# Kernel optimization log

Measured on AMD Instinct MI355X. Metric: run time of the kernel, lower is better.

## Reference

```python
import jax, jax.numpy as jnp
import numpy as np

S, B, H, V, T = 128, 64, 512, 100, 32  # src_len, batch, hidden, vocab, tgt_len


def setup_inputs() -> dict:
    key = jax.random.key(0)
    ks = jax.random.split(key, 12)
    sc = 0.05
    return {
        "encoder_outputs": jax.random.normal(ks[0], (S, B, H), jnp.float32),
        "W_emb": jax.random.normal(ks[1], (V, H), jnp.float32) * sc,   # embedding.weight.T (Linear(V->H, no bias) on one-hot)
        "W_comb": jax.random.normal(ks[2], (H, 2 * H), jnp.float32) * sc,
        "b_comb": jnp.zeros((H,), jnp.float32),
        "W_ih": jax.random.normal(ks[3], (3 * H, H), jnp.float32) * sc,
        "W_hh": jax.random.normal(ks[4], (3 * H, H), jnp.float32) * sc,
        "b_ih": jnp.zeros((3 * H,), jnp.float32),
        "b_hh": jnp.zeros((3 * H,), jnp.float32),
        "W_out": jax.random.normal(ks[5], (V, H), jnp.float32) * sc,
        "b_out": jnp.zeros((V,), jnp.float32),
        "w_vat": jax.random.normal(ks[6], (H,), jnp.float32) * sc,     # vat: Linear(H->1)
        "b_vat": jnp.zeros((), jnp.float32),
        "target_seq": jax.random.randint(ks[7], (T, B), 0, V),
    }


def reference(encoder_outputs, W_emb, W_comb, b_comb, W_ih, W_hh, b_ih, b_hh,
              W_out, b_out, w_vat, b_vat, target_seq):
    # train_forward with teacher forcing, dropout in eval (identity).
    def step(h, sym):  # h: [B,H], sym: [B] int
        embedded = W_emb[sym]                                   # one-hot @ embedding.weight.T
        # Bahdanau additive attention: scores over src positions
        scores = jnp.tanh(encoder_outputs + h[None]) @ w_vat + b_vat   # [S,B]
        attn = jax.nn.softmax(scores, axis=0)                   # softmax over S
        ctx = jnp.einsum('sb,sbh->bh', attn, encoder_outputs)   # [B,H]
        x = jax.nn.relu(jnp.concatenate([embedded, ctx], axis=-1) @ W_comb.T + b_comb)
        # PyTorch GRU cell
        gi = x @ W_ih.T + b_ih                                   # [B,3H]
        gh = h @ W_hh.T + b_hh
        ir, iz, inn = jnp.split(gi, 3, axis=-1)
        hr, hz, hn = jnp.split(gh, 3, axis=-1)
        r = jax.nn.sigmoid(ir + hr)
        z = jax.nn.sigmoid(iz + hz)
        n = jnp.tanh(inn + r * hn)
        h_new = (1.0 - z) * n + z * h
        logits = jax.nn.log_softmax(h_new @ W_out.T + b_out, axis=-1)  # [B,V]
        return h_new, logits

    h0 = jnp.zeros((encoder_outputs.shape[1], W_hh.shape[1]), encoder_outputs.dtype)
    _, logits = jax.lax.scan(step, h0, target_seq[:-1])          # [T-1,B,V]
    return jnp.transpose(logits, (1, 0, 2))                      # [B,T-1,V]
```

## Files before the change

### kernel.cpp

```cpp
#include <hip/hip_runtime.h>
#include <hip/hip_fp16.h>

#define Sn 128
#define Bn 64
#define Hn 512
#define Vn 100
#define TSn 31

typedef unsigned int   u32;
typedef unsigned short u16;
typedef _Float16 f16x2 __attribute__((ext_vector_type(2)));

#define OFF_ENC2  0ull
#define OFF_WEMB  8388608ull
#define OFF_WCOMB 8491008ull
#define OFF_WIH   9539584ull
#define OFF_WHH   11112448ull
#define OFF_WOUT  12685312ull
#define OFF_XEX   12787712ull
#define OFF_HEX   12853248ull
#define OFF_HHEX  12984320ull
#define OFF_PLOG  13049856ull
#define OFF_CNT   13152256ull

__device__ __forceinline__ u16 f2h(float f){ _Float16 h=(_Float16)f; return __builtin_bit_cast(u16,h); }
__device__ __forceinline__ f16x2 uh2(u32 u){ return __builtin_bit_cast(f16x2,u); }
__device__ __forceinline__ float2 h2f(u32 u){ f16x2 h=uh2(u); return make_float2((float)h.x,(float)h.y); }
__device__ __forceinline__ u32 pack2h(float a, float b){ return (u32)f2h(a) | ((u32)f2h(b) << 16); }

#if __has_builtin(__builtin_amdgcn_fdot2)
__device__ __forceinline__ float dot2acc(u32 a, u32 b, float acc){
    return __builtin_amdgcn_fdot2(uh2(a), uh2(b), acc, false);
}
#else
__device__ __forceinline__ float dot2acc(u32 a, u32 b, float acc){
    float2 x=h2f(a), y=h2f(b); return acc + x.x*y.x + x.y*y.y;
}
#endif

__device__ __forceinline__ float dot8h(uint4 w, uint4 v, float acc){
    acc = dot2acc(w.x, v.x, acc); acc = dot2acc(w.y, v.y, acc);
    acc = dot2acc(w.z, v.z, acc); acc = dot2acc(w.w, v.w, acc);
    return acc;
}

__device__ __forceinline__ float fast_tanh(float x){
    float e = __expf(2.0f*x);
    return 1.0f - 2.0f/(e + 1.0f);
}
__device__ __forceinline__ float fast_sigmoid(float x){ return 1.0f/(1.0f + __expf(-x)); }

__device__ __forceinline__ float wave_sum(float v){
#pragma unroll
    for (int o = 32; o; o >>= 1) v += __shfl_xor(v, o);
    return v;
}
__device__ __forceinline__ float wave_max(float v){
#pragma unroll
    for (int o = 32; o; o >>= 1) v = fmaxf(v, __shfl_xor(v, o));
    return v;
}

__device__ __forceinline__ void sib_barrier(u32* cnt, u32 target){
    asm volatile("s_waitcnt vmcnt(0)" ::: "memory");
    __syncthreads();
    if (threadIdx.x == 0) {
        __hip_atomic_fetch_add(cnt, 1u, __ATOMIC_RELAXED, __HIP_MEMORY_SCOPE_AGENT);
        u32 v;
        do {
            __builtin_amdgcn_s_sleep(2);
            v = __hip_atomic_load(cnt, __ATOMIC_RELAXED, __HIP_MEMORY_SCOPE_AGENT);
        } while (v < target);
    }
    __syncthreads();
}

#define CONV(S,D,N)                                              \
    for (int i = t0; i < (N)/4; i += stride) {                   \
        float4 v = ((const float4*)(S))[i];                      \
        ushort4 o;                                               \
        o.x = f2h(v.x); o.y = f2h(v.y);                          \
        o.z = f2h(v.z); o.w = f2h(v.w);                          \
        ((ushort4*)(D))[i] = o;                                  \
    }

__global__ __launch_bounds__(256) void conv_f16(
    const float* __restrict__ enc, const float* __restrict__ Wemb,
    const float* __restrict__ Wcomb, const float* __restrict__ Wih,
    const float* __restrict__ Whh, const float* __restrict__ Wout,
    char* __restrict__ ws)
{
    const int t0 = blockIdx.x*256 + threadIdx.x;
    const int stride = gridDim.x*256;
    if (blockIdx.x == 0 && threadIdx.x < 128) ((u32*)(ws + OFF_CNT))[threadIdx.x] = 0;

    {
        u16* de = (u16*)(ws + OFF_ENC2);
        for (int c = t0; c < Sn*Bn*Hn/4; c += stride) {
            const int h4 = c & 127;
            const int s  = (c >> 7) & 127;
            const int bb = c >> 14;
            float4 v = ((const float4*)enc)[(s*Bn + bb)*(Hn/4) + h4];
            ushort4 o;
            o.x = f2h(v.x); o.y = f2h(v.y); o.z = f2h(v.z); o.w = f2h(v.w);
            ((ushort4*)de)[c] = o;
        }
    }
    u16* dm = (u16*)(ws + OFF_WEMB);
    u16* dc = (u16*)(ws + OFF_WCOMB);
    u16* di = (u16*)(ws + OFF_WIH);
    u16* dh = (u16*)(ws + OFF_WHH);
    u16* doo = (u16*)(ws + OFF_WOUT);
    CONV(Wemb, dm, Vn*Hn)
    CONV(Wcomb,dc, Hn*2*Hn)
    CONV(Wih,  di, 3*Hn*Hn)
    CONV(Whh,  dh, 3*Hn*Hn)
    CONV(Wout, doo, Vn*Hn)
}

__global__ __launch_bounds__(1024) void bahdanau_decoder(
    const float* __restrict__ bcomb, const float* __restrict__ bih,
    const float* __restrict__ bhh, const float* __restrict__ bout,
    const float* __restrict__ wvat, const float* __restrict__ bvat,
    const int* __restrict__ tgt, float* __restrict__ out, char* __restrict__ ws)
{
    const u16* Wemb_h  = (const u16*)(ws + OFF_WEMB);
    const u16* Wcomb_h = (const u16*)(ws + OFF_WCOMB);
    const u16* Wih_h   = (const u16*)(ws + OFF_WIH);
    const u16* Whh_h   = (const u16*)(ws + OFF_WHH);
    const u16* Wout_h  = (const u16*)(ws + OFF_WOUT);
    u32* cntA = (u32*)(ws + OFF_CNT);
    u32* cntB = cntA + 64;

    extern __shared__ __align__(16) u16 enc_lds[];
    __shared__ __align__(16) float h_full[Hn];
    __shared__ __align__(16) u16   hh_full[Hn];
    __shared__ __align__(16) u16   ec_s[2*Hn];
    __shared__ __align__(16) u16   x_s[Hn];
    __shared__ __align__(16) float scores_s[Sn];
    __shared__ __align__(16) float attnw_s[Sn];
    __shared__ __align__(16) float2 pctx[4][256];
    __shared__ __align__(16) float plog_s[112];
    __shared__ __align__(16) u16   hn16_stage[128];

    const int tid  = threadIdx.x;
    const int lane = tid & 63;
    const int wid  = tid >> 6;
    const int bid  = blockIdx.x;
    const int xcd  = bid & 7;
    const int lb   = bid >> 3;
    const int q    = xcd & 3;
    const int b    = 2*lb + (xcd >> 2);
    const int j0   = q*128;

    {
        const uint4* src = (const uint4*)(ws + OFF_ENC2 + (size_t)b*Sn*Hn*2);
        for (int i = tid; i < Sn*Hn/8; i += 1024) ((uint4*)enc_lds)[i] = src[i];
    }
    if (tid < Hn) { h_full[tid] = 0.0f; hh_full[tid] = 0; }
    const float4 Wa = ((const float4*)wvat)[2*lane];
    const float4 Wb = ((const float4*)wvat)[2*lane+1];
    const float bv = bvat[0];
    __syncthreads();

    for (int t = 0; t < TSn; ++t) {
        const u32 tgtc = 4u*(t+1);

        for (int s = wid; s < Sn; s += 16) {
            const uint4 E = ((const uint4*)(enc_lds + s*Hn))[lane];
            const float4 Ha = ((const float4*)h_full)[2*lane];
            const float4 Hb = ((const float4*)h_full)[2*lane+1];
            const float2 e0 = h2f(E.x), e1 = h2f(E.y), e2 = h2f(E.z), e3 = h2f(E.w);
            float acc = fast_tanh(e0.x+Ha.x)*Wa.x + fast_tanh(e0.y+Ha.y)*Wa.y
                      + fast_tanh(e1.x+Ha.z)*Wa.z + fast_tanh(e1.y+Ha.w)*Wa.w
                      + fast_tanh(e2.x+Hb.x)*Wb.x + fast_tanh(e2.y+Hb.y)*Wb.y
                      + fast_tanh(e3.x+Hb.z)*Wb.z + fast_tanh(e3.y+Hb.w)*Wb.w;
            acc = wave_sum(acc);
            if (lane == 0) scores_s[s] = acc + bv;
        }
        __syncthreads();

        if (wid == 0) {
            const float s0 = scores_s[lane], s1 = scores_s[lane+64];
            const float mx = wave_max(fmaxf(s0, s1));
            const float e0 = __expf(s0-mx), e1 = __expf(s1-mx);
            const float inv = 1.0f / wave_sum(e0 + e1);
            attnw_s[lane]    = e0 * inv;
            attnw_s[lane+64] = e1 * inv;
        } else if (wid == 1) {
            const int sym = tgt[t*Bn + b];
            ((uint4*)ec_s)[lane] = ((const uint4*)(Wemb_h + (size_t)sym*Hn))[lane];
        }
        __syncthreads();

        {
            const int op = tid & 255;
            const int sc = tid >> 8;
            float2 acc = make_float2(0.f, 0.f);
#pragma unroll 8
            for (int k = 0; k < 32; ++k) {
                const int s = sc*32 + k;
                const float2 ef = h2f(*(const u32*)(enc_lds + s*Hn + 2*op));
                const float a = attnw_s[s];
                acc.x += a*ef.x; acc.y += a*ef.y;
            }
            pctx[sc][op] = acc;
        }
        __syncthreads();
        if (tid < 256) {
            float2 c0 = pctx[0][tid], c1 = pctx[1][tid], c2 = pctx[2][tid], c3 = pctx[3][tid];
            ((u32*)(ec_s + Hn))[tid] = pack2h(c0.x+c1.x+c2.x+c3.x, c0.y+c1.y+c2.y+c3.y);
        }
        __syncthreads();

        for (int jj = wid; jj < 128; jj += 16) {
            const int j = j0 + jj;
            const uint4* row = (const uint4*)(Wcomb_h + (size_t)j*2*Hn);
            const uint4 w0 = row[lane], w1 = row[64+lane];
            const uint4 e0 = ((const uint4*)ec_s)[lane], e1 = ((const uint4*)ec_s)[64+lane];
            float acc = dot8h(w1, e1, dot8h(w0, e0, 0.0f));
            acc = wave_sum(acc);
            if (lane == 0) x_s[j] = f2h(fmaxf(acc + bcomb[j], 0.0f));
        }
        __syncthreads();
        if (wid == 0)
            ((volatile u32*)(ws + OFF_XEX))[b*256 + q*64 + lane] = ((u32*)x_s)[q*64 + lane];
        sib_barrier(cntA + b, tgtc);
        if (wid < 3) {
            const int qq = (q + 1 + wid) & 3;
            ((u32*)x_s)[qq*64 + lane] = ((const volatile u32*)(ws + OFF_XEX))[b*256 + qq*64 + lane];
        }
        __syncthreads();

        for (int jj = wid; jj < 128; jj += 16) {
            const int j = j0 + jj;
            const uint4 Wr = ((const uint4*)(Wih_h + (size_t)j*Hn))[lane];
            const uint4 Wz = ((const uint4*)(Wih_h + (size_t)(Hn + j)*Hn))[lane];
            const uint4 Wn = ((const uint4*)(Wih_h + (size_t)(2*Hn + j)*Hn))[lane];
            const uint4 Ur = ((const uint4*)(Whh_h + (size_t)j*Hn))[lane];
            const uint4 Uz = ((const uint4*)(Whh_h + (size_t)(Hn + j)*Hn))[lane];
            const uint4 Un = ((const uint4*)(Whh_h + (size_t)(2*Hn + j)*Hn))[lane];
            const uint4 Xv = ((const uint4*)x_s)[lane];
            const uint4 Hv = ((const uint4*)hh_full)[lane];
            float gr = dot8h(Ur, Hv, dot8h(Wr, Xv, 0.0f));
            float gz = dot8h(Uz, Hv, dot8h(Wz, Xv, 0.0f));
            float an = dot8h(Wn, Xv, 0.0f);
            float cn = dot8h(Un, Hv, 0.0f);
            gr = wave_sum(gr); gz = wave_sum(gz);
            an = wave_sum(an); cn = wave_sum(cn);
            if (lane == 0) {
                const float r = fast_sigmoid(gr + bih[j]      + bhh[j]);
                const float z = fast_sigmoid(gz + bih[Hn+j]   + bhh[Hn+j]);
                const float n = fast_tanh(an + bih[2*Hn+j] + r*(cn + bhh[2*Hn+j]));
                const float hv = (1.0f - z)*n + z*h_full[j];
                h_full[j] = hv;
                hn16_stage[jj] = f2h(hv);
            }
        }
        __syncthreads();

        for (int v = wid; v < Vn; v += 16) {
            const u32 w = *(const u32*)(Wout_h + (size_t)v*Hn + j0 + 2*lane);
            const u32 hh = ((u32*)hn16_stage)[lane];
            float acc = dot2acc(w, hh, 0.0f);
            acc = wave_sum(acc);
            if (lane == 0) plog_s[v] = acc;
        }
        __syncthreads();

        if (wid == 0) {
            if (lane < 50) {
                volatile float* pp = (volatile float*)(ws + OFF_PLOG) + ((size_t)b*4 + q)*100;
                pp[2*lane]   = plog_s[2*lane];
                pp[2*lane+1] = plog_s[2*lane+1];
            }
        } else if (wid == 1) {
            volatile float* hp = (volatile float*)(ws + OFF_HEX) + (size_t)b*Hn + j0;
            hp[2*lane]   = h_full[j0 + 2*lane];
            hp[2*lane+1] = h_full[j0 + 2*lane + 1];
        } else if (wid == 2) {
            ((volatile u32*)(ws + OFF_HHEX))[b*256 + q*64 + lane] = ((u32*)hn16_stage)[lane];
        }
        sib_barrier(cntB + b, tgtc);
        if (wid < 3) {
            const int qq = (q + 1 + wid) & 3;
            const volatile float* hp = (const volatile float*)(ws + OFF_HEX) + (size_t)b*Hn + qq*128;
            h_full[qq*128 + 2*lane]     = hp[2*lane];
            h_full[qq*128 + 2*lane + 1] = hp[2*lane+1];
            ((u32*)hh_full)[qq*64 + lane] = ((const volatile u32*)(ws + OFF_HHEX))[b*256 + qq*64 + lane];
        } else if (wid == 3) {
            ((u32*)hh_full)[q*64 + lane] = ((u32*)hn16_stage)[lane];
        } else if (wid == 4 && q == 0) {
            float a0 = 0.f, a1 = 0.f;
            if (lane < 50) {
                a0 = plog_s[2*lane] + bout[2*lane];
                a1 = plog_s[2*lane+1] + bout[2*lane+1];
#pragma unroll
                for (int qq = 1; qq < 4; ++qq) {
                    const volatile float* pp = (const volatile float*)(ws + OFF_PLOG) + ((size_t)b*4 + qq)*100;
                    a0 += pp[2*lane];
                    a1 += pp[2*lane+1];
                }
            }
            const float l0 = (lane < 50) ? a0 : -3.0e38f;
            const float l1 = (lane < 50) ? a1 : -3.0e38f;
            const float mx = wave_max(fmaxf(l0, l1));
            const float e0 = (lane < 50) ? __expf(l0-mx) : 0.0f;
            const float e1 = (lane < 50) ? __expf(l1-mx) : 0.0f;
            const float lse = mx + __logf(wave_sum(e0 + e1));
            float* op = out + ((size_t)b*TSn + t)*Vn;
            if (lane < 50) { op[2*lane] = l0 - lse; op[2*lane+1] = l1 - lse; }
        }
        __syncthreads();
    }
}

extern "C" void kernel_launch(void* const* d_in, const int* in_sizes, int n_in,
                              void* d_out, int out_size, void* d_ws, size_t ws_size,
                              hipStream_t stream) {
    const float* enc   = (const float*)d_in[0];
    const float* Wemb  = (const float*)d_in[1];
    const float* Wcomb = (const float*)d_in[2];
    const float* bcomb = (const float*)d_in[3];
    const float* Wih   = (const float*)d_in[4];
    const float* Whh   = (const float*)d_in[5];
    const float* bih   = (const float*)d_in[6];
    const float* bhh   = (const float*)d_in[7];
    const float* Wout  = (const float*)d_in[8];
    const float* bout  = (const float*)d_in[9];
    const float* wvat  = (const float*)d_in[10];
    const float* bvat  = (const float*)d_in[11];
    const int*   tgt   = (const int*)d_in[12];
    float* out = (float*)d_out;
    char*  ws  = (char*)d_ws;

    conv_f16<<<1024, 256, 0, stream>>>(enc, Wemb, Wcomb, Wih, Whh, Wout, ws);

    void* args[] = { &bcomb, &bih, &bhh, &bout, &wvat, &bvat, &tgt, &out, &ws };
    hipLaunchCooperativeKernel((const void*)bahdanau_decoder,
                               dim3(256), dim3(1024), args, (size_t)(Sn*Hn*2), stream);
}
```

Before: 1.218 ms.

## Precompute embedding-combine table and overlap W_hh gates with sibling barrier

Folds the embedding half of W_comb into a precomputed fp32 table, Wemb projected through W_comb, built by a new prep kernel, so each step only does a 512-wide context dot plus a table lookup. Splits the sibling barrier into arrive and wait, and computes the W_hh·h gate dot products between them so that work overlaps the cross-block wait. Also pads the counters onto separate cache lines, uses relaxed atomics instead of volatile for exchange traffic, and shortens the spin sleep. This adds an extra prep kernel and more register pressure from the held gate partials.

```diff
diff --git a/kernel.cpp b/kernel.cpp
--- a/kernel.cpp
+++ b/kernel.cpp
@@ -12,16 +12,16 @@
 typedef _Float16 f16x2 __attribute__((ext_vector_type(2)));
 
 #define OFF_ENC2  0ull
-#define OFF_WEMB  8388608ull
-#define OFF_WCOMB 8491008ull
-#define OFF_WIH   9539584ull
-#define OFF_WHH   11112448ull
-#define OFF_WOUT  12685312ull
-#define OFF_XEX   12787712ull
-#define OFF_HEX   12853248ull
-#define OFF_HHEX  12984320ull
-#define OFF_PLOG  13049856ull
-#define OFF_CNT   13152256ull
+#define OFF_WC2   8388608ull
+#define OFF_WIH   8912896ull
+#define OFF_WHH   10485760ull
+#define OFF_WOUT  12058624ull
+#define OFF_EMB2  12161024ull
+#define OFF_XEX   12365824ull
+#define OFF_HEXF  12431360ull
+#define OFF_HEXH  12562432ull
+#define OFF_PLOG  12627968ull
+#define OFF_CNT   12730368ull
 
 __device__ __forceinline__ u16 f2h(float f){ _Float16 h=(_Float16)f; return __builtin_bit_cast(u16,h); }
 __device__ __forceinline__ f16x2 uh2(u32 u){ return __builtin_bit_cast(f16x2,u); }
@@ -61,16 +61,29 @@
     return v;
 }
 
-__device__ __forceinline__ void sib_barrier(u32* cnt, u32 target){
+__device__ __forceinline__ void ast(u32* p, u32 v){
+    __hip_atomic_store(p, v, __ATOMIC_RELAXED, __HIP_MEMORY_SCOPE_AGENT);
+}
+__device__ __forceinline__ u32 ald(u32* p){
+    return __hip_atomic_load(p, __ATOMIC_RELAXED, __HIP_MEMORY_SCOPE_AGENT);
+}
+__device__ __forceinline__ void astf(float* p, float v){
+    __hip_atomic_store((u32*)p, __builtin_bit_cast(u32, v), __ATOMIC_RELAXED, __HIP_MEMORY_SCOPE_AGENT);
+}
+__device__ __forceinline__ float aldf(float* p){
+    return __builtin_bit_cast(float, __hip_atomic_load((u32*)p, __ATOMIC_RELAXED, __HIP_MEMORY_SCOPE_AGENT));
+}
+
+__device__ __forceinline__ void sib_arrive(u32* cnt){
     asm volatile("s_waitcnt vmcnt(0)" ::: "memory");
     __syncthreads();
+    if (threadIdx.x == 0)
+        __hip_atomic_fetch_add(cnt, 1u, __ATOMIC_RELAXED, __HIP_MEMORY_SCOPE_AGENT);
+}
+__device__ __forceinline__ void sib_wait(u32* cnt, u32 target){
     if (threadIdx.x == 0) {
-        __hip_atomic_fetch_add(cnt, 1u, __ATOMIC_RELAXED, __HIP_MEMORY_SCOPE_AGENT);
-        u32 v;
-        do {
-            __builtin_amdgcn_s_sleep(2);
-            v = __hip_atomic_load(cnt, __ATOMIC_RELAXED, __HIP_MEMORY_SCOPE_AGENT);
-        } while (v < target);
+        while (__hip_atomic_load(cnt, __ATOMIC_RELAXED, __HIP_MEMORY_SCOPE_AGENT) < target)
+            __builtin_amdgcn_s_sleep(1);
     }
     __syncthreads();
 }
@@ -84,16 +97,13 @@
         ((ushort4*)(D))[i] = o;                                  \
     }
 
-__global__ __launch_bounds__(256) void conv_f16(
-    const float* __restrict__ enc, const float* __restrict__ Wemb,
-    const float* __restrict__ Wcomb, const float* __restrict__ Wih,
-    const float* __restrict__ Whh, const float* __restrict__ Wout,
-    char* __restrict__ ws)
+__global__ __launch_bounds__(256) void prep_conv(
+    const float* __restrict__ enc, const float* __restrict__ Wcomb,
+    const float* __restrict__ Wih, const float* __restrict__ Whh,
+    const float* __restrict__ Wout, char* __restrict__ ws)
 {
     const int t0 = blockIdx.x*256 + threadIdx.x;
     const int stride = gridDim.x*256;
-    if (blockIdx.x == 0 && threadIdx.x < 128) ((u32*)(ws + OFF_CNT))[threadIdx.x] = 0;
-
     {
         u16* de = (u16*)(ws + OFF_ENC2);
         for (int c = t0; c < Sn*Bn*Hn/4; c += stride) {
@@ -106,16 +116,45 @@
             ((ushort4*)de)[c] = o;
         }
     }
-    u16* dm = (u16*)(ws + OFF_WEMB);
-    u16* dc = (u16*)(ws + OFF_WCOMB);
-    u16* di = (u16*)(ws + OFF_WIH);
-    u16* dh = (u16*)(ws + OFF_WHH);
-    u16* doo = (u16*)(ws + OFF_WOUT);
-    CONV(Wemb, dm, Vn*Hn)
-    CONV(Wcomb,dc, Hn*2*Hn)
-    CONV(Wih,  di, 3*Hn*Hn)
-    CONV(Whh,  dh, 3*Hn*Hn)
-    CONV(Wout, doo, Vn*Hn)
+    {
+        u16* dc = (u16*)(ws + OFF_WC2);
+        for (int i = t0; i < Hn*Hn/4; i += stride) {
+            const int j = i >> 7, kk = i & 127;
+            float4 v = ((const float4*)Wcomb)[j*256 + 128 + kk];
+            ushort4 o;
+            o.x = f2h(v.x); o.y = f2h(v.y); o.z = f2h(v.z); o.w = f2h(v.w);
+            ((ushort4*)dc)[i] = o;
+        }
+    }
+    CONV(Wih,  (u16*)(ws+OFF_WIH),  3*Hn*Hn)
+    CONV(Whh,  (u16*)(ws+OFF_WHH),  3*Hn*Hn)
+    CONV(Wout, (u16*)(ws+OFF_WOUT), Vn*Hn)
+    u32* cnt = (u32*)(ws + OFF_CNT);
+    for (int i = t0; i < 64*2*16; i += stride) cnt[i] = 0u;
+}
+
+__global__ __launch_bounds__(512) void prep_emb2(
+    const float* __restrict__ Wemb, const float* __restrict__ Wcomb,
+    char* __restrict__ ws)
+{
+    float* EMB2 = (float*)(ws + OFF_EMB2);
+    const int w = threadIdx.x >> 6;
+    const int lane = threadIdx.x & 63;
+    const int j = blockIdx.x*8 + w;
+    const float4* wc = (const float4*)(Wcomb + (size_t)j*2*Hn);
+#pragma unroll
+    for (int pass = 0; pass < 2; ++pass) {
+        const int v = lane + 64*pass;
+        if (v < Vn) {
+            const float4* we = (const float4*)(Wemb + (size_t)v*Hn);
+            float acc = 0.0f;
+            for (int k4 = 0; k4 < 128; ++k4) {
+                const float4 a = wc[k4], b = we[k4];
+                acc += a.x*b.x + a.y*b.y + a.z*b.z + a.w*b.w;
+            }
+            EMB2[(size_t)v*Hn + j] = acc;
+        }
+    }
 }
 
 __global__ __launch_bounds__(1024) void bahdanau_decoder(
@@ -124,24 +163,28 @@
     const float* __restrict__ wvat, const float* __restrict__ bvat,
     const int* __restrict__ tgt, float* __restrict__ out, char* __restrict__ ws)
 {
-    const u16* Wemb_h  = (const u16*)(ws + OFF_WEMB);
-    const u16* Wcomb_h = (const u16*)(ws + OFF_WCOMB);
-    const u16* Wih_h   = (const u16*)(ws + OFF_WIH);
-    const u16* Whh_h   = (const u16*)(ws + OFF_WHH);
-    const u16* Wout_h  = (const u16*)(ws + OFF_WOUT);
-    u32* cntA = (u32*)(ws + OFF_CNT);
-    u32* cntB = cntA + 64;
+    const u16* WC2  = (const u16*)(ws + OFF_WC2);
+    const u16* WIH  = (const u16*)(ws + OFF_WIH);
+    const u16* WHH  = (const u16*)(ws + OFF_WHH);
+    const u16* WOUT = (const u16*)(ws + OFF_WOUT);
+    const float* EMB2 = (const float*)(ws + OFF_EMB2);
+    u32*   XEX  = (u32*)(ws + OFF_XEX);
+    float* HEXF = (float*)(ws + OFF_HEXF);
+    u32*   HEXH = (u32*)(ws + OFF_HEXH);
+    float* PLOG = (float*)(ws + OFF_PLOG);
+    u32*   CNT  = (u32*)(ws + OFF_CNT);
 
     extern __shared__ __align__(16) u16 enc_lds[];
     __shared__ __align__(16) float h_full[Hn];
-    __shared__ __align__(16) u16   hh_full[Hn];
-    __shared__ __align__(16) u16   ec_s[2*Hn];
-    __shared__ __align__(16) u16   x_s[Hn];
+    __shared__ __align__(16) u32   hh32[Hn/2];
+    __shared__ __align__(16) u32   ctx32[Hn/2];
+    __shared__ __align__(16) u32   x32[Hn/2];
+    __shared__ __align__(16) u16   xst[128];
+    __shared__ __align__(16) u16   hn16[128];
     __shared__ __align__(16) float scores_s[Sn];
     __shared__ __align__(16) float attnw_s[Sn];
-    __shared__ __align__(16) float2 pctx[4][256];
+    __shared__ __align__(16) float2 pctx_s[4][256];
     __shared__ __align__(16) float plog_s[112];
-    __shared__ __align__(16) u16   hn16_stage[128];
 
     const int tid  = threadIdx.x;
     const int lane = tid & 63;
@@ -152,12 +195,15 @@
     const int q    = xcd & 3;
     const int b    = 2*lb + (xcd >> 2);
     const int j0   = q*128;
+    u32* cntA = CNT + (b*2 + 0)*16;
+    u32* cntB = CNT + (b*2 + 1)*16;
 
     {
         const uint4* src = (const uint4*)(ws + OFF_ENC2 + (size_t)b*Sn*Hn*2);
         for (int i = tid; i < Sn*Hn/8; i += 1024) ((uint4*)enc_lds)[i] = src[i];
     }
-    if (tid < Hn) { h_full[tid] = 0.0f; hh_full[tid] = 0; }
+    if (tid < Hn) h_full[tid] = 0.0f;
+    if (tid < Hn/2) hh32[tid] = 0u;
     const float4 Wa = ((const float4*)wvat)[2*lane];
     const float4 Wb = ((const float4*)wvat)[2*lane+1];
     const float bv = bvat[0];
@@ -166,17 +212,19 @@
     for (int t = 0; t < TSn; ++t) {
         const u32 tgtc = 4u*(t+1);
 
-        for (int s = wid; s < Sn; s += 16) {
-            const uint4 E = ((const uint4*)(enc_lds + s*Hn))[lane];
+        {
             const float4 Ha = ((const float4*)h_full)[2*lane];
             const float4 Hb = ((const float4*)h_full)[2*lane+1];
-            const float2 e0 = h2f(E.x), e1 = h2f(E.y), e2 = h2f(E.z), e3 = h2f(E.w);
-            float acc = fast_tanh(e0.x+Ha.x)*Wa.x + fast_tanh(e0.y+Ha.y)*Wa.y
-                      + fast_tanh(e1.x+Ha.z)*Wa.z + fast_tanh(e1.y+Ha.w)*Wa.w
-                      + fast_tanh(e2.x+Hb.x)*Wb.x + fast_tanh(e2.y+Hb.y)*Wb.y
-                      + fast_tanh(e3.x+Hb.z)*Wb.z + fast_tanh(e3.y+Hb.w)*Wb.w;
-            acc = wave_sum(acc);
-            if (lane == 0) scores_s[s] = acc + bv;
+            for (int s = wid; s < Sn; s += 16) {
+                const uint4 E = ((const uint4*)(enc_lds + s*Hn))[lane];
+                const float2 e0 = h2f(E.x), e1 = h2f(E.y), e2 = h2f(E.z), e3 = h2f(E.w);
+                float acc = fast_tanh(e0.x+Ha.x)*Wa.x + fast_tanh(e0.y+Ha.y)*Wa.y
+                          + fast_tanh(e1.x+Ha.z)*Wa.z + fast_tanh(e1.y+Ha.w)*Wa.w
+                          + fast_tanh(e2.x+Hb.x)*Wb.x + fast_tanh(e2.y+Hb.y)*Wb.y
+                          + fast_tanh(e3.x+Hb.z)*Wb.z + fast_tanh(e3.y+Hb.w)*Wb.w;
+                acc = wave_sum(acc);
+                if (lane == 0) scores_s[s] = acc + bv;
+            }
         }
         __syncthreads();
 
@@ -187,126 +235,140 @@
             const float inv = 1.0f / wave_sum(e0 + e1);
             attnw_s[lane]    = e0 * inv;
             attnw_s[lane+64] = e1 * inv;
-        } else if (wid == 1) {
+        }
+        __syncthreads();
+
+        {
+            const int op = tid & 255, sc = tid >> 8;
+            float ax = 0.0f, ay = 0.0f;
+#pragma unroll 8
+            for (int i2 = 0; i2 < 32; ++i2) {
+                const int s = sc*32 + i2;
+                const float a = attnw_s[s];
+                const float2 ef = h2f(((const u32*)(enc_lds + s*Hn))[op]);
+                ax += a*ef.x; ay += a*ef.y;
+            }
+            pctx_s[sc][op] = make_float2(ax, ay);
+        }
+        __syncthreads();
+        if (tid < 256) {
+            const float2 c0 = pctx_s[0][tid], c1 = pctx_s[1][tid];
+            const float2 c2 = pctx_s[2][tid], c3 = pctx_s[3][tid];
+            ctx32[tid] = pack2h(c0.x+c1.x+c2.x+c3.x, c0.y+c1.y+c2.y+c3.y);
+        }
+        __syncthreads();
+
+        {
             const int sym = tgt[t*Bn + b];
-            ((uint4*)ec_s)[lane] = ((const uint4*)(Wemb_h + (size_t)sym*Hn))[lane];
-        }
-        __syncthreads();
-
-        {
-            const int op = tid & 255;
-            const int sc = tid >> 8;
-            float2 acc = make_float2(0.f, 0.f);
-#pragma unroll 8
-            for (int k = 0; k < 32; ++k) {
-                const int s = sc*32 + k;
-                const float2 ef = h2f(*(const u32*)(enc_lds + s*Hn + 2*op));
-                const float a = attnw_s[s];
-                acc.x += a*ef.x; acc.y += a*ef.y;
-            }
-            pctx[sc][op] = acc;
-        }
-        __syncthreads();
-        if (tid < 256) {
-            float2 c0 = pctx[0][tid], c1 = pctx[1][tid], c2 = pctx[2][tid], c3 = pctx[3][tid];
-            ((u32*)(ec_s + Hn))[tid] = pack2h(c0.x+c1.x+c2.x+c3.x, c0.y+c1.y+c2.y+c3.y);
-        }
-        __syncthreads();
-
-        for (int jj = wid; jj < 128; jj += 16) {
-            const int j = j0 + jj;
-            const uint4* row = (const uint4*)(Wcomb_h + (size_t)j*2*Hn);
-            const uint4 w0 = row[lane], w1 = row[64+lane];
-            const uint4 e0 = ((const uint4*)ec_s)[lane], e1 = ((const uint4*)ec_s)[64+lane];
-            float acc = dot8h(w1, e1, dot8h(w0, e0, 0.0f));
-            acc = wave_sum(acc);
-            if (lane == 0) x_s[j] = f2h(fmaxf(acc + bcomb[j], 0.0f));
+            const uint4 C = ((const uint4*)ctx32)[lane];
+            for (int jj = wid; jj < 128; jj += 16) {
+                const int j = j0 + jj;
+                const uint4 W = ((const uint4*)(WC2 + (size_t)j*Hn))[lane];
+                float acc = dot8h(W, C, 0.0f);
+                acc = wave_sum(acc);
+                if (lane == 0)
+                    xst[jj] = f2h(fmaxf(acc + EMB2[(size_t)sym*Hn + j] + bcomb[j], 0.0f));
+            }
         }
         __syncthreads();
         if (wid == 0)
-            ((volatile u32*)(ws + OFF_XEX))[b*256 + q*64 + lane] = ((u32*)x_s)[q*64 + lane];
-        sib_barrier(cntA + b, tgtc);
+            ast(XEX + b*256 + q*64 + lane, (u32)xst[2*lane] | ((u32)xst[2*lane+1] << 16));
+        sib_arrive(cntA);
+
+        float ghr[8], ghz[8], ghn[8];
+        {
+            const uint4 HH = ((const uint4*)hh32)[lane];
+#pragma unroll
+            for (int k = 0; k < 8; ++k) {
+                const int j = j0 + wid*8 + k;
+                const uint4 R = ((const uint4*)(WHH + (size_t)j*Hn))[lane];
+                const uint4 Z = ((const uint4*)(WHH + (size_t)(Hn + j)*Hn))[lane];
+                const uint4 N = ((const uint4*)(WHH + (size_t)(2*Hn + j)*Hn))[lane];
+                ghr[k] = wave_sum(dot8h(R, HH, 0.0f));
+                ghz[k] = wave_sum(dot8h(Z, HH, 0.0f));
+                ghn[k] = wave_sum(dot8h(N, HH, 0.0f));
+            }
+        }
+        sib_wait(cntA, tgtc);
+
         if (wid < 3) {
             const int qq = (q + 1 + wid) & 3;
-            ((u32*)x_s)[qq*64 + lane] = ((const volatile u32*)(ws + OFF_XEX))[b*256 + qq*64 + lane];
-        }
-        __syncthreads();
-
-        for (int jj = wid; jj < 128; jj += 16) {
-            const int j = j0 + jj;
-            const uint4 Wr = ((const uint4*)(Wih_h + (size_t)j*Hn))[lane];
-            const uint4 Wz = ((const uint4*)(Wih_h + (size_t)(Hn + j)*Hn))[lane];
-            const uint4 Wn = ((const uint4*)(Wih_h + (size_t)(2*Hn + j)*Hn))[lane];
-            const uint4 Ur = ((const uint4*)(Whh_h + (size_t)j*Hn))[lane];
-            const uint4 Uz = ((const uint4*)(Whh_h + (size_t)(Hn + j)*Hn))[lane];
-            const uint4 Un = ((const uint4*)(Whh_h + (size_t)(2*Hn + j)*Hn))[lane];
-            const uint4 Xv = ((const uint4*)x_s)[lane];
-            const uint4 Hv = ((const uint4*)hh_full)[lane];
-            float gr = dot8h(Ur, Hv, dot8h(Wr, Xv, 0.0f));
-            float gz = dot8h(Uz, Hv, dot8h(Wz, Xv, 0.0f));
-            float an = dot8h(Wn, Xv, 0.0f);
-            float cn = dot8h(Un, Hv, 0.0f);
-            gr = wave_sum(gr); gz = wave_sum(gz);
-            an = wave_sum(an); cn = wave_sum(cn);
-            if (lane == 0) {
-                const float r = fast_sigmoid(gr + bih[j]      + bhh[j]);
-                const float z = fast_sigmoid(gz + bih[Hn+j]   + bhh[Hn+j]);
-                const float n = fast_tanh(an + bih[2*Hn+j] + r*(cn + bhh[2*Hn+j]));
-                const float hv = (1.0f - z)*n + z*h_full[j];
-                h_full[j] = hv;
-                hn16_stage[jj] = f2h(hv);
-            }
-        }
-        __syncthreads();
-
-        for (int v = wid; v < Vn; v += 16) {
-            const u32 w = *(const u32*)(Wout_h + (size_t)v*Hn + j0 + 2*lane);
-            const u32 hh = ((u32*)hn16_stage)[lane];
-            float acc = dot2acc(w, hh, 0.0f);
-            acc = wave_sum(acc);
-            if (lane == 0) plog_s[v] = acc;
+            x32[qq*64 + lane] = ald(XEX + b*256 + qq*64 + lane);
+        } else if (wid == 3) {
+            x32[q*64 + lane] = (u32)xst[2*lane] | ((u32)xst[2*lane+1] << 16);
+        }
+        __syncthreads();
+
+        {
+            const uint4 X = ((const uint4*)x32)[lane];
+#pragma unroll
+            for (int k = 0; k < 8; ++k) {
+                const int j = j0 + wid*8 + k;
+                const uint4 R = ((const uint4*)(WIH + (size_t)j*Hn))[lane];
+                const uint4 Z = ((const uint4*)(WIH + (size_t)(Hn + j)*Hn))[lane];
+                const uint4 N = ((const uint4*)(WIH + (size_t)(2*Hn + j)*Hn))[lane];
+                const float gir = wave_sum(dot8h(R, X, 0.0f));
+                const float giz = wave_sum(dot8h(Z, X, 0.0f));
+                const float gin = wave_sum(dot8h(N, X, 0.0f));
+                if (lane == 0) {
+                    const float r = fast_sigmoid(gir + ghr[k] + bih[j] + bhh[j]);
+                    const float z = fast_sigmoid(giz + ghz[k] + bih[Hn+j] + bhh[Hn+j]);
+                    const float n = fast_tanh(gin + bih[2*Hn+j] + r*(ghn[k] + bhh[2*Hn+j]));
+                    const float hv = (1.0f - z)*n + z*h_full[j];
+                    h_full[j] = hv;
+                    hn16[wid*8 + k] = f2h(hv);
+                }
+            }
+        }
+        __syncthreads();
+
+        {
+            const u32 hh = ((const u32*)hn16)[lane];
+            for (int v = wid; v < Vn; v += 16) {
+                const u32 w = ((const u32*)(WOUT + (size_t)v*Hn + j0))[lane];
+                const float acc = wave_sum(dot2acc(w, hh, 0.0f));
+                if (lane == 0) plog_s[v] = acc;
+            }
         }
         __syncthreads();
 
         if (wid == 0) {
             if (lane < 50) {
-                volatile float* pp = (volatile float*)(ws + OFF_PLOG) + ((size_t)b*4 + q)*100;
-                pp[2*lane]   = plog_s[2*lane];
-                pp[2*lane+1] = plog_s[2*lane+1];
+                astf(PLOG + ((size_t)b*4 + q)*100 + 2*lane,     plog_s[2*lane]);
+                astf(PLOG + ((size_t)b*4 + q)*100 + 2*lane + 1, plog_s[2*lane+1]);
             }
         } else if (wid == 1) {
-            volatile float* hp = (volatile float*)(ws + OFF_HEX) + (size_t)b*Hn + j0;
-            hp[2*lane]   = h_full[j0 + 2*lane];
-            hp[2*lane+1] = h_full[j0 + 2*lane + 1];
+            astf(HEXF + (size_t)b*Hn + j0 + 2*lane,     h_full[j0 + 2*lane]);
+            astf(HEXF + (size_t)b*Hn + j0 + 2*lane + 1, h_full[j0 + 2*lane + 1]);
         } else if (wid == 2) {
-            ((volatile u32*)(ws + OFF_HHEX))[b*256 + q*64 + lane] = ((u32*)hn16_stage)[lane];
-        }
-        sib_barrier(cntB + b, tgtc);
+            ast(HEXH + b*256 + q*64 + lane, (u32)hn16[2*lane] | ((u32)hn16[2*lane+1] << 16));
+        }
+        sib_arrive(cntB);
+        sib_wait(cntB, tgtc);
+
         if (wid < 3) {
             const int qq = (q + 1 + wid) & 3;
-            const volatile float* hp = (const volatile float*)(ws + OFF_HEX) + (size_t)b*Hn + qq*128;
-            h_full[qq*128 + 2*lane]     = hp[2*lane];
-            h_full[qq*128 + 2*lane + 1] = hp[2*lane+1];
-            ((u32*)hh_full)[qq*64 + lane] = ((const volatile u32*)(ws + OFF_HHEX))[b*256 + qq*64 + lane];
+            h_full[qq*128 + 2*lane]     = aldf(HEXF + (size_t)b*Hn + qq*128 + 2*lane);
+            h_full[qq*128 + 2*lane + 1] = aldf(HEXF + (size_t)b*Hn + qq*128 + 2*lane + 1);
+            hh32[qq*64 + lane] = ald(HEXH + b*256 + qq*64 + lane);
         } else if (wid == 3) {
-            ((u32*)hh_full)[q*64 + lane] = ((u32*)hn16_stage)[lane];
+            hh32[q*64 + lane] = (u32)hn16[2*lane] | ((u32)hn16[2*lane+1] << 16);
         } else if (wid == 4 && q == 0) {
-            float a0 = 0.f, a1 = 0.f;
+            float a0 = 0.0f, a1 = 0.0f;
             if (lane < 50) {
-                a0 = plog_s[2*lane] + bout[2*lane];
-                a1 = plog_s[2*lane+1] + bout[2*lane+1];
-#pragma unroll
-                for (int qq = 1; qq < 4; ++qq) {
-                    const volatile float* pp = (const volatile float*)(ws + OFF_PLOG) + ((size_t)b*4 + qq)*100;
-                    a0 += pp[2*lane];
-                    a1 += pp[2*lane+1];
+                a0 = bout[2*lane];
+                a1 = bout[2*lane+1];
+#pragma unroll
+                for (int qq = 0; qq < 4; ++qq) {
+                    a0 += aldf(PLOG + ((size_t)b*4 + qq)*100 + 2*lane);
+                    a1 += aldf(PLOG + ((size_t)b*4 + qq)*100 + 2*lane + 1);
                 }
             }
             const float l0 = (lane < 50) ? a0 : -3.0e38f;
             const float l1 = (lane < 50) ? a1 : -3.0e38f;
             const float mx = wave_max(fmaxf(l0, l1));
-            const float e0 = (lane < 50) ? __expf(l0-mx) : 0.0f;
-            const float e1 = (lane < 50) ? __expf(l1-mx) : 0.0f;
+            const float e0 = (lane < 50) ? __expf(l0 - mx) : 0.0f;
+            const float e1 = (lane < 50) ? __expf(l1 - mx) : 0.0f;
             const float lse = mx + __logf(wave_sum(e0 + e1));
             float* op = out + ((size_t)b*TSn + t)*Vn;
             if (lane < 50) { op[2*lane] = l0 - lse; op[2*lane+1] = l1 - lse; }
@@ -334,7 +396,8 @@
     float* out = (float*)d_out;
     char*  ws  = (char*)d_ws;
 
-    conv_f16<<<1024, 256, 0, stream>>>(enc, Wemb, Wcomb, Wih, Whh, Wout, ws);
+    prep_conv<<<512, 256, 0, stream>>>(enc, Wcomb, Wih, Whh, Wout, ws);
+    prep_emb2<<<64, 512, 0, stream>>>(Wemb, Wcomb, ws);
 
     void* args[] = { &bcomb, &bih, &bhh, &bout, &wvat, &bvat, &tgt, &out, &ws };
     hipLaunchCooperativeKernel((const void*)bahdanau_decoder,
```

New measurement: 2.129 ms. 74.8% more time.
